# Performance work log

Hardware: AMD Instinct MI355X
Metric: run time of the kernel (lower is better)

Reference implementation:

```python
import jax, jax.numpy as jnp
import numpy as np

N_NODES = 100000
N_EDGES = 500000
FEAT = 128
HID = 256
N_ETYPES = 249
N_LINKS = 16384


def _lin_init(key, out_dim, in_dim, bias=True):
    k1, k2 = jax.random.split(key)
    bound = 1.0 / np.sqrt(in_dim)
    w = jax.random.uniform(k1, (out_dim, in_dim), jnp.float32, -bound, bound)
    if bias:
        b = jax.random.uniform(k2, (out_dim,), jnp.float32, -bound, bound)
        return w, b
    return w


def setup_inputs() -> dict:
    key = jax.random.key(0)
    ks = jax.random.split(key, 24)
    x = jax.random.normal(ks[0], (N_NODES, FEAT), jnp.float32)
    edge_index = jax.random.randint(ks[1], (2, N_EDGES), 0, N_NODES, jnp.int64)
    edge_type = jax.random.randint(ks[2], (N_EDGES,), 0, N_ETYPES, jnp.int64)
    src_idx = jax.random.randint(ks[3], (N_LINKS,), 0, N_NODES, jnp.int64)
    dst_idx = jax.random.randint(ks[4], (N_LINKS,), 0, N_NODES, jnp.int64)

    w_emb, b_emb = _lin_init(ks[5], HID, FEAT)
    edge_table = jax.random.normal(ks[6], (N_ETYPES, HID), jnp.float32)
    wl0, bl0 = _lin_init(ks[7], HID, HID)
    wr0 = _lin_init(ks[8], HID, HID, bias=False)
    we0, be0 = _lin_init(ks[9], HID, HID)
    wl1, bl1 = _lin_init(ks[10], HID, HID)
    wr1 = _lin_init(ks[11], HID, HID, bias=False)
    we1, be1 = _lin_init(ks[12], HID, HID)
    wp1, bp1 = _lin_init(ks[13], HID, 4 * HID)
    wp2, bp2 = _lin_init(ks[14], 1, HID)
    return dict(x=x, edge_index=edge_index, edge_type=edge_type,
                src_idx=src_idx, dst_idx=dst_idx,
                w_emb=w_emb, b_emb=b_emb, edge_table=edge_table,
                wl0=wl0, bl0=bl0, wr0=wr0, we0=we0, be0=be0,
                wl1=wl1, bl1=bl1, wr1=wr1, we1=we1, be1=be1,
                wp1=wp1, bp1=bp1, wp2=wp2, bp2=bp2)


def _sage_layer(h, src, dst, deg, wl, bl, wr):
    # mean aggregation over incoming edges + self loop (add_self_loops)
    nb_sum = jax.ops.segment_sum(h[src], dst, num_segments=N_NODES)  # [N,H]
    mean = (nb_sum + h) / (deg + 1.0)[:, None]
    return mean @ wl.T + bl + h @ wr.T  # lin_l(mean) + lin_r(x)


def reference(x, edge_index, edge_type, src_idx, dst_idx,
              w_emb, b_emb, edge_table,
              wl0, bl0, wr0, we0, be0,
              wl1, bl1, wr1, we1, be1,
              wp1, bp1, wp2, bp2):
    src, dst = edge_index[0], edge_index[1]
    deg = jax.ops.segment_sum(jnp.ones((src.shape[0],), jnp.float32), dst,
                              num_segments=N_NODES)  # in-degree (no self loop)
    h = x @ w_emb.T + b_emb  # node_embedding
    edge_emb = edge_table[edge_type]  # [E,H]
    # edge_lin outputs are discarded by SAGEConv (matches torch behavior)
    _ = edge_emb @ we0.T + be0
    _ = edge_emb @ we1.T + be1
    h = jax.nn.relu(_sage_layer(h, src, dst, deg, wl0, bl0, wr0))
    h = jax.nn.relu(_sage_layer(h, src, dst, deg, wl1, bl1, wr1))
    s, d = h[src_idx], h[dst_idx]
    combined = jnp.concatenate([s, d, s * d, jnp.abs(s - d)], axis=1)  # [B,4H]
    hidden = jax.nn.relu(combined @ wp1.T + bp1)
    logits = hidden @ wp2.T + bp2  # [B,1]
    return jax.nn.sigmoid(logits).squeeze()
```

## Files before the change

### kernel.cpp

```cpp
#include <hip/hip_runtime.h>
#include <hip/hip_bf16.h>
#include <cstdint>
#include <type_traits>

#define N_NODES 100000
#define N_EDGES 500000
#define FEAT 128
#define HID 256
#define N_LINKS 16384
#define BCAP 32

typedef __attribute__((ext_vector_type(8))) short short8;
typedef __attribute__((ext_vector_type(4))) float floatx4;
typedef __attribute__((ext_vector_type(16))) float floatx16;

__device__ __forceinline__ float ldf(const float* p) { return *p; }
__device__ __forceinline__ float ldf(const __hip_bfloat16* p) { return __bfloat162float(*p); }
__device__ __forceinline__ void stf(float* p, float v) { *p = v; }
__device__ __forceinline__ void stf(__hip_bfloat16* p, float v) { *p = __float2bfloat16(v); }

__device__ __forceinline__ void load4(const __hip_bfloat16* p, float v[4]) {
    const uint2 q = *(const uint2*)p;
    v[0] = __uint_as_float(q.x << 16);
    v[1] = __uint_as_float(q.x & 0xffff0000u);
    v[2] = __uint_as_float(q.y << 16);
    v[3] = __uint_as_float(q.y & 0xffff0000u);
}
__device__ __forceinline__ void store4(__hip_bfloat16* p, const float v[4]) {
    __hip_bfloat16 b[4];
    b[0] = __float2bfloat16(v[0]); b[1] = __float2bfloat16(v[1]);
    b[2] = __float2bfloat16(v[2]); b[3] = __float2bfloat16(v[3]);
    *(uint2*)p = *(const uint2*)b;
}

__device__ __forceinline__ void load8(const __hip_bfloat16* p, float v[8]) {
    const uint4 q = *(const uint4*)p;
    v[0] = __uint_as_float(q.x << 16);
    v[1] = __uint_as_float(q.x & 0xffff0000u);
    v[2] = __uint_as_float(q.y << 16);
    v[3] = __uint_as_float(q.y & 0xffff0000u);
    v[4] = __uint_as_float(q.z << 16);
    v[5] = __uint_as_float(q.z & 0xffff0000u);
    v[6] = __uint_as_float(q.w << 16);
    v[7] = __uint_as_float(q.w & 0xffff0000u);
}
__device__ __forceinline__ void store8(__hip_bfloat16* p, const float v[8]) {
    __hip_bfloat16 b[8];
    #pragma unroll
    for (int i = 0; i < 8; i++) b[i] = __float2bfloat16(v[i]);
    *(uint4*)p = *(const uint4*)b;
}

__device__ __forceinline__ void acc8(const uint4& q, float a[8]) {
    a[0] += __uint_as_float(q.x << 16);
    a[1] += __uint_as_float(q.x & 0xffff0000u);
    a[2] += __uint_as_float(q.y << 16);
    a[3] += __uint_as_float(q.y & 0xffff0000u);
    a[4] += __uint_as_float(q.z << 16);
    a[5] += __uint_as_float(q.z & 0xffff0000u);
    a[6] += __uint_as_float(q.w << 16);
    a[7] += __uint_as_float(q.w & 0xffff0000u);
}

__device__ __forceinline__ void gload_lds16(const short* g, short* lds) {
    __builtin_amdgcn_global_load_lds(
        reinterpret_cast<const __attribute__((address_space(1))) unsigned int*>(
            reinterpret_cast<uintptr_t>(g)),
        reinterpret_cast<__attribute__((address_space(3))) unsigned int*>(
            reinterpret_cast<uintptr_t>(lds)),
        16, 0, 0);
}

__device__ __forceinline__ int clampi(int v, int n) { return ((unsigned)v < (unsigned)n) ? v : 0; }


__global__ void zero_f32(float* p, int n) {
    int i = blockIdx.x * blockDim.x + threadIdx.x;
    if (i < n) p[i] = 0.0f;
}

__global__ void init_misc(int* __restrict__ deg, int* __restrict__ h0pad,
                          int* __restrict__ h1pad) {
    int i = blockIdx.x * blockDim.x + threadIdx.x;
    if (i < N_NODES) deg[i] = 0;
    if (i < 128) { h0pad[i] = 0; h1pad[i] = 0; }
}

__global__ void cvt_x(const float4* __restrict__ x, __hip_bfloat16* __restrict__ xb, int n4) {
    int i = blockIdx.x * blockDim.x + threadIdx.x;
    if (i >= n4) return;
    float4 v = x[i];
    float a[4] = {v.x, v.y, v.z, v.w};
    store4(&xb[(size_t)i * 4], a);
}

#define POF_EMB 0
#define POF_L0  32768
#define POF_R0  98304
#define POF_L1  163840
#define POF_R1  229376
#define WP_TOTAL 294912
#define WP1_N   262144
__global__ void cvt_wall(const float* __restrict__ w_emb, const float* __restrict__ wl0,
                         const float* __restrict__ wr0, const float* __restrict__ wl1,
                         const float* __restrict__ wr1, const float* __restrict__ wp1,
                         __hip_bfloat16* __restrict__ wbp, __hip_bfloat16* __restrict__ wbp1) {
    int i = blockIdx.x * blockDim.x + threadIdx.x;
    if (i < WP_TOTAL) {
        const float* src; int off, ks;
        if      (i < POF_L0) { src = w_emb; off = POF_EMB; ks = 128; }
        else if (i < POF_R0) { src = wl0;   off = POF_L0;  ks = 256; }
        else if (i < POF_L1) { src = wr0;   off = POF_R0;  ks = 256; }
        else if (i < POF_R1) { src = wl1;   off = POF_L1;  ks = 256; }
        else                 { src = wr1;   off = POF_R1;  ks = 256; }
        int o = i - off;
        int kseg = o >> 11;
        int rem  = o & 2047;
        int n = rem >> 3, j = rem & 7;
        wbp[i] = __float2bfloat16(src[n * ks + kseg * 8 + j]);
    } else if (i < WP_TOTAL + WP1_N) {
        int j = i - WP_TOTAL;
        wbp1[j] = __float2bfloat16(wp1[j]);
    }
}


__global__ void fill_buckets(const int* __restrict__ src, const int* __restrict__ dst,
                             int* __restrict__ deg, int* __restrict__ ebuf, int nE) {
    int e = blockIdx.x * blockDim.x + threadIdx.x;
    if (e >= nE) return;
    int d = clampi(dst[e], N_NODES);
    int pos = atomicAdd(&deg[d], 1);
    if (pos < BCAP) ebuf[d * BCAP + pos] = clampi(src[e], N_NODES);
}

__global__ void sort_rows(const int* __restrict__ deg, int* __restrict__ ebuf) {
    int n = blockIdx.x * blockDim.x + threadIdx.x;
    if (n >= N_NODES) return;
    int dg = deg[n]; if (dg > BCAP) dg = BCAP;
    int start = n * BCAP, end = start + dg;
    for (int i = start + 1; i < end; i++) {
        int key = ebuf[i];
        int j = i - 1;
        while (j >= start && ebuf[j] > key) { ebuf[j + 1] = ebuf[j]; j--; }
        ebuf[j + 1] = key;
    }
}


__global__ __launch_bounds__(256) void gather_agg(const __hip_bfloat16* __restrict__ h,
                                                  const int* __restrict__ deg,
                                                  const int* __restrict__ ebuf,
                                                  __hip_bfloat16* __restrict__ agg) {
    int wave = threadIdx.x >> 6, lane = threadIdx.x & 63;
    int half = lane >> 5, l32 = lane & 31;
    int n = blockIdx.x * 8 + wave * 2 + half;
    bool active = (n < N_NODES);
    int nn = active ? n : 0;
    int dg = active ? deg[nn] : 0;
    int dgc = dg > BCAP ? BCAP : dg;
    int start = nn * BCAP;
    int end = start + dgc;

    float acc[8];
    {
        float sv[8];
        load8(&h[(long long)nn * HID + l32 * 8], sv);
        #pragma unroll
        for (int k = 0; k < 8; k++) acc[k] = sv[k];
    }

    for (int e = start; e < end; e += 8) {
        int cnt = end - e;
        uint4 raw[8];
        #pragma unroll
        for (int i = 0; i < 8; i++) {
            int t = e + i; t = (t < end) ? t : (end - 1);
            int idx = ebuf[t];
            int s = (i < cnt) ? idx : N_NODES;
            raw[i] = *(const uint4*)&h[(long long)s * HID + l32 * 8];
        }
        #pragma unroll
        for (int i = 0; i < 8; i++) acc8(raw[i], acc);
    }

    float inv = 1.0f / (float)(dg + 1);
    #pragma unroll
    for (int k = 0; k < 8; k++) acc[k] *= inv;
    if (active) store8(&agg[(long long)n * HID + l32 * 8], acc);
}


template <int KS, bool DUAL, typename TC, bool RELU>
__global__ __launch_bounds__(256, 2) void gemm_kc(const __hip_bfloat16* __restrict__ A1,
                                                  const __hip_bfloat16* __restrict__ A2,
                                                  const __hip_bfloat16* __restrict__ Bp1,
                                                  const __hip_bfloat16* __restrict__ Bp2,
                                                  const float* __restrict__ bias,
                                                  TC* __restrict__ C, int M, int GX) {
    const int N = 256;
    const int NSTEP = (DUAL ? 2 : 1) * KS / 64;
    __shared__ __align__(16) short As[2][128 * 64];
    __shared__ __align__(16) short Bs[2][64 * 128];

    const int tid = threadIdx.x;
    const int w = tid >> 6, lane = tid & 63;
    const int half = lane >> 5, l32 = lane & 31;
    const int cg = blockIdx.y;

    const short* A1s = (const short*)A1;
    const short* A2s = (const short*)A2;
    const short* B1s = (const short*)Bp1;
    const short* B2s = (const short*)Bp2;

    const int NT = (M + 127) / 128;
    for (int tile = blockIdx.x; tile < NT; tile += GX) {
        const int row0 = tile * 128;

        auto stage = [&](int buf, int t) {
            const short* Asrc; const short* Bsrc; int kl;
            if (!DUAL || t < KS / 64) { Asrc = A1s; Bsrc = B1s; kl = t * 64; }
            else                      { Asrc = A2s; Bsrc = B2s; kl = t * 64 - KS; }
            #pragma unroll
            for (int i = 0; i < 4; i++) {
                int idx = i * 256 + tid;
                int row = idx >> 3, b16 = idx & 7;
                int gr = row0 + row; if (gr >= M) gr = M - 1;
                gload_lds16(Asrc + (size_t)gr * KS + kl + ((b16 ^ (row & 7)) * 8),
                            (short*)&As[buf][idx * 8]);
            }
            #pragma unroll
            for (int i = 0; i < 4; i++) {
                int idx = i * 256 + tid;
                int kseg = idx >> 7, col = idx & 127;
                gload_lds16(Bsrc + ((size_t)((kl >> 3) + kseg) * 256 + cg * 128 + col) * 8,
                            (short*)&Bs[buf][idx * 8]);
            }
        };

        floatx16 acc[4] = {};
        int cur = 0;
        stage(0, 0);
        __syncthreads();

        for (int t = 0; t < NSTEP; t++) {
            if (t + 1 < NSTEP) stage(cur ^ 1, t + 1);

            const int arow = w * 32 + l32;
            #pragma unroll
            for (int k16 = 0; k16 < 4; k16++) {
                int e = k16 * 2 + half;
                short8 a = *(const short8*)&As[cur][(arow * 8 + (e ^ (l32 & 7))) * 8];
                #pragma unroll
                for (int ct = 0; ct < 4; ct++) {
                    short8 b = *(const short8*)&Bs[cur][(e * 128 + ct * 32 + l32) * 8];
                    acc[ct] = __builtin_amdgcn_mfma_f32_32x32x16_bf16(a, b, acc[ct], 0, 0, 0);
                }
            }
            __syncthreads();
            cur ^= 1;
        }

        #pragma unroll
        for (int ct = 0; ct < 4; ct++) {
            int c = cg * 128 + ct * 32 + l32;
            float bc = bias[c];
            #pragma unroll
            for (int reg = 0; reg < 16; reg++) {
                int rr = row0 + w * 32 + (reg & 3) + 8 * (reg >> 2) + 4 * half;
                if (rr < M) {
                    float v = acc[ct][reg] + bc;
                    if (RELU) v = fmaxf(v, 0.0f);
                    stf(&C[(size_t)rr * N + c], v);
                }
            }
        }
    }
}


__device__ __forceinline__ short8 comb_frag(const __hip_bfloat16* __restrict__ h,
                                            int srow, int drow, int ka) {
    int seg = ka >> 8, off = ka & 255;
    const __hip_bfloat16* ps = &h[(size_t)srow * HID + off];
    const __hip_bfloat16* pd = &h[(size_t)drow * HID + off];
    if (seg == 0) return *(const short8*)ps;
    if (seg == 1) return *(const short8*)pd;
    float s[8], d[8];
    load8(ps, s);
    load8(pd, d);
    __hip_bfloat16 b[8];
    if (seg == 2) {
        #pragma unroll
        for (int j = 0; j < 8; j++) b[j] = __float2bfloat16(s[j] * d[j]);
    } else {
        #pragma unroll
        for (int j = 0; j < 8; j++) b[j] = __float2bfloat16(fabsf(s[j] - d[j]));
    }
    return *(const short8*)b;
}

template <int RT>
__global__ __launch_bounds__(256, 2) void pred_gemm(const __hip_bfloat16* __restrict__ h,
                                                    const int* __restrict__ src_idx,
                                                    const int* __restrict__ dst_idx,
                                                    const __hip_bfloat16* __restrict__ B1,
                                                    const float* __restrict__ bias,
                                                    float* __restrict__ C, int M, int K) {
    const int N = 256;
    const int SZ = 4 * 256 * 8;
    __shared__ __align__(16) short Bs[2][SZ];

    int w = threadIdx.x >> 6, lane = threadIdx.x & 63;
    int quad = lane >> 4, l16 = lane & 15;
    int wr = w >> 1, wc = w & 1;
    const int WROWS = RT * 16;
    int row0 = blockIdx.x * (2 * WROWS) + wr * WROWS;
    int colbase = wc * 128;

    const short* B1s = (const short*)B1;

    floatx4 acc[RT][8] = {};

    int r[RT], sidx[RT], didx[RT];
    #pragma unroll
    for (int i = 0; i < RT; i++) {
        int rr = row0 + i * 16 + l16;
        r[i] = rr < M ? rr : M - 1;
        sidx[i] = clampi(src_idx[r[i]], N_NODES);
        didx[i] = clampi(dst_idx[r[i]], N_NODES);
    }
    int scol = threadIdx.x;
    int ldsoff = (w * 64) * 8;

    short8 a1c[RT], a1n[RT];

    #pragma unroll
    for (int q = 0; q < 4; q++)
        gload_lds16(B1s + (size_t)scol * K + q * 8, &Bs[0][q * 256 * 8 + ldsoff]);
    {
        int ka = quad * 8;
        #pragma unroll
        for (int i = 0; i < RT; i++)
            a1c[i] = comb_frag(h, sidx[i], didx[i], ka);
    }
    __syncthreads();

    const int NK = K / 32;
    int cur = 0;
    for (int k = 0; k < NK; k++) {
        if (k + 1 < NK) {
            int k0n = (k + 1) * 32;
            #pragma unroll
            for (int q = 0; q < 4; q++)
                gload_lds16(B1s + (size_t)scol * K + k0n + q * 8,
                            &Bs[cur ^ 1][q * 256 * 8 + ldsoff]);
            int ka = k0n + quad * 8;
            #pragma unroll
            for (int i = 0; i < RT; i++)
                a1n[i] = comb_frag(h, sidx[i], didx[i], ka);
        }

        short8 b1[8];
        #pragma unroll
        for (int ct = 0; ct < 8; ct++) {
            int col = colbase + ct * 16 + l16;
            b1[ct] = *(const short8*)&Bs[cur][(quad * 256 + col) * 8];
        }
        #pragma unroll
        for (int i = 0; i < RT; i++)
            #pragma unroll
            for (int ct = 0; ct < 8; ct++)
                acc[i][ct] = __builtin_amdgcn_mfma_f32_16x16x32_bf16(a1c[i], b1[ct], acc[i][ct], 0, 0, 0);
        __syncthreads();
        cur ^= 1;
        #pragma unroll
        for (int i = 0; i < RT; i++) a1c[i] = a1n[i];
    }

    #pragma unroll
    for (int rt = 0; rt < RT; rt++) {
        #pragma unroll
        for (int ct = 0; ct < 8; ct++) {
            int c = colbase + ct * 16 + l16;
            float bc = bias[c];
            #pragma unroll
            for (int i = 0; i < 4; i++) {
                int rr = row0 + rt * 16 + quad * 4 + i;
                if (rr < M) {
                    float v = acc[rt][ct][i] + bc;
                    v = fmaxf(v, 0.0f);
                    C[(size_t)rr * N + c] = v;
                }
            }
        }
    }
}

__global__ __launch_bounds__(256) void pred_final(const float* __restrict__ hidden,
                                                  const float* __restrict__ wp2,
                                                  const float* __restrict__ bp2,
                                                  float* __restrict__ out) {
    int wave = threadIdx.x >> 6;
    int lane = threadIdx.x & 63;
    int row = blockIdx.x * 4 + wave;
    if (row >= N_LINKS) return;
    const float4 hv = *(const float4*)&hidden[(long long)row * HID + lane * 4];
    const float4 wv = *(const float4*)&wp2[lane * 4];
    float v = hv.x * wv.x + hv.y * wv.y + hv.z * wv.z + hv.w * wv.w;
    #pragma unroll
    for (int off = 32; off > 0; off >>= 1) v += __shfl_down(v, off, 64);
    if (lane == 0) out[row] = 1.0f / (1.0f + expf(-(v + bp2[0])));
}


extern "C" void kernel_launch(void* const* d_in, const int* in_sizes, int n_in,
                              void* d_out, int out_size, void* d_ws, size_t ws_size,
                              hipStream_t stream) {
    const float* x          = (const float*)d_in[0];
    const int*   edge_index = (const int*)d_in[1];
    const int*   e_src      = edge_index;
    const int*   e_dst      = edge_index + N_EDGES;
    const int*   src_idx    = (const int*)d_in[3];
    const int*   dst_idx    = (const int*)d_in[4];
    const float* w_emb      = (const float*)d_in[5];
    const float* b_emb      = (const float*)d_in[6];
    const float* wl0        = (const float*)d_in[8];
    const float* bl0        = (const float*)d_in[9];
    const float* wr0        = (const float*)d_in[10];
    const float* wl1        = (const float*)d_in[13];
    const float* bl1        = (const float*)d_in[14];
    const float* wr1        = (const float*)d_in[15];
    const float* wp1        = (const float*)d_in[18];
    const float* bp1        = (const float*)d_in[19];
    const float* wp2        = (const float*)d_in[20];
    const float* bp2        = (const float*)d_in[21];
    float* out = (float*)d_out;

    typedef __hip_bfloat16 bf16;
    const size_t NH  = (size_t)N_NODES * HID;
    const size_t NH1 = (size_t)(N_NODES + 1) * HID;

    char* p = (char*)d_ws;
    bf16* h0   = (bf16*)p;  p += NH1 * 2;
    bf16* h1   = (bf16*)p;  p += NH1 * 2;
    bf16* agg  = (bf16*)p;  p += NH * 2;
    bf16* xb   = (bf16*)p;  p += (size_t)N_NODES * FEAT * 2;
    bf16* wbp  = (bf16*)p;  p += (size_t)WP_TOTAL * 2;
    bf16* wbp1 = (bf16*)p;  p += (size_t)WP1_N * 2;
    p = (char*)(((uintptr_t)p + 255) & ~(uintptr_t)255);
    int* deg  = (int*)p; p += (size_t)N_NODES * 4;
    int* ebuf = (int*)p; p += (size_t)N_NODES * BCAP * 4;
    const size_t need = (size_t)(p - (char*)d_ws);

    if (ws_size < need) {
        zero_f32<<<(out_size + 255) / 256, 256, 0, stream>>>(out, out_size);
        return;
    }

    float* hidden = (float*)h1;

    init_misc<<<(N_NODES + 255) / 256, 256, 0, stream>>>(
        deg, (int*)(h0 + NH), (int*)(h1 + NH));
    fill_buckets<<<(N_EDGES + 255) / 256, 256, 0, stream>>>(e_src, e_dst, deg, ebuf, N_EDGES);
    sort_rows<<<(N_NODES + 255) / 256, 256, 0, stream>>>(deg, ebuf);

    cvt_x<<<((N_NODES * FEAT / 4) + 255) / 256, 256, 0, stream>>>((const float4*)x, xb, N_NODES * FEAT / 4);
    cvt_wall<<<((WP_TOTAL + WP1_N) + 255) / 256, 256, 0, stream>>>(
        w_emb, wl0, wr0, wl1, wr1, wp1, wbp, wbp1);

    const int GX = 256;
    dim3 pgrid(GX, 2);

    gemm_kc<128, false, bf16, false><<<pgrid, 256, 0, stream>>>(
        xb, nullptr, wbp + POF_EMB, nullptr, b_emb, h0, N_NODES, GX);

    gather_agg<<<(N_NODES + 7) / 8, 256, 0, stream>>>(h0, deg, ebuf, agg);
    gemm_kc<256, true, bf16, true><<<pgrid, 256, 0, stream>>>(
        agg, h0, wbp + POF_L0, wbp + POF_R0, bl0, h1, N_NODES, GX);

    gather_agg<<<(N_NODES + 7) / 8, 256, 0, stream>>>(h1, deg, ebuf, agg);
    gemm_kc<256, true, bf16, true><<<pgrid, 256, 0, stream>>>(
        agg, h1, wbp + POF_L1, wbp + POF_R1, bl1, h0, N_NODES, GX);

    pred_gemm<2><<<(N_LINKS + 63) / 64, 256, 0, stream>>>(
        h0, src_idx, dst_idx, wbp1, bp1, hidden, N_LINKS, 4 * HID);
    pred_final<<<N_LINKS / 4, 256, 0, stream>>>(hidden, wp2, bp2, out);
}
```

Before: 460.2 us.

## Repack predictor weights k-segmented and split pred_gemm across column groups

The predictor weight wp1 is now converted into the same k-segmented bf16 packed layout as the other weights, so each B stage becomes one coalesced 16-byte load per thread. pred_gemm is re-tiled: each block covers 64 rows by 64 columns, with a second grid dimension over four column groups and one 16-row tile per wave. This raises the block count from 256 to 1024, cuts LDS per block, and allows higher occupancy. The cost is that the gathered combined-feature A fragments are recomputed four times, once per column group.

Measured after the change: 468.3 us. About the same (+1.8%).

```diff
diff --git a/kernel.cpp b/kernel.cpp
--- a/kernel.cpp
+++ b/kernel.cpp
@@ -99,29 +99,26 @@
 #define POF_R0  98304
 #define POF_L1  163840
 #define POF_R1  229376
-#define WP_TOTAL 294912
-#define WP1_N   262144
+#define POF_P1  294912
+#define WP_ALL  557056
 __global__ void cvt_wall(const float* __restrict__ w_emb, const float* __restrict__ wl0,
                          const float* __restrict__ wr0, const float* __restrict__ wl1,
                          const float* __restrict__ wr1, const float* __restrict__ wp1,
-                         __hip_bfloat16* __restrict__ wbp, __hip_bfloat16* __restrict__ wbp1) {
+                         __hip_bfloat16* __restrict__ wbp) {
     int i = blockIdx.x * blockDim.x + threadIdx.x;
-    if (i < WP_TOTAL) {
-        const float* src; int off, ks;
-        if      (i < POF_L0) { src = w_emb; off = POF_EMB; ks = 128; }
-        else if (i < POF_R0) { src = wl0;   off = POF_L0;  ks = 256; }
-        else if (i < POF_L1) { src = wr0;   off = POF_R0;  ks = 256; }
-        else if (i < POF_R1) { src = wl1;   off = POF_L1;  ks = 256; }
-        else                 { src = wr1;   off = POF_R1;  ks = 256; }
-        int o = i - off;
-        int kseg = o >> 11;
-        int rem  = o & 2047;
-        int n = rem >> 3, j = rem & 7;
-        wbp[i] = __float2bfloat16(src[n * ks + kseg * 8 + j]);
-    } else if (i < WP_TOTAL + WP1_N) {
-        int j = i - WP_TOTAL;
-        wbp1[j] = __float2bfloat16(wp1[j]);
-    }
+    if (i >= WP_ALL) return;
+    const float* src; int off, ks;
+    if      (i < POF_L0) { src = w_emb; off = POF_EMB; ks = 128; }
+    else if (i < POF_R0) { src = wl0;   off = POF_L0;  ks = 256; }
+    else if (i < POF_L1) { src = wr0;   off = POF_R0;  ks = 256; }
+    else if (i < POF_R1) { src = wl1;   off = POF_L1;  ks = 256; }
+    else if (i < POF_P1) { src = wr1;   off = POF_R1;  ks = 256; }
+    else                 { src = wp1;   off = POF_P1;  ks = 1024; }
+    int o = i - off;
+    int kseg = o >> 11;
+    int rem  = o & 2047;
+    int n = rem >> 3, j = rem & 7;
+    wbp[i] = __float2bfloat16(src[n * ks + kseg * 8 + j]);
 }
 
 
@@ -300,99 +297,66 @@
     return *(const short8*)b;
 }
 
-template <int RT>
-__global__ __launch_bounds__(256, 2) void pred_gemm(const __hip_bfloat16* __restrict__ h,
+
+__global__ __launch_bounds__(256, 4) void pred_gemm(const __hip_bfloat16* __restrict__ h,
                                                     const int* __restrict__ src_idx,
                                                     const int* __restrict__ dst_idx,
-                                                    const __hip_bfloat16* __restrict__ B1,
+                                                    const __hip_bfloat16* __restrict__ Bp,
                                                     const float* __restrict__ bias,
-                                                    float* __restrict__ C, int M, int K) {
+                                                    float* __restrict__ C, int M) {
     const int N = 256;
-    const int SZ = 4 * 256 * 8;
-    __shared__ __align__(16) short Bs[2][SZ];
+    const int K = 1024;
+    __shared__ __align__(16) short Bs[2][4 * 64 * 8];
 
     int w = threadIdx.x >> 6, lane = threadIdx.x & 63;
     int quad = lane >> 4, l16 = lane & 15;
-    int wr = w >> 1, wc = w & 1;
-    const int WROWS = RT * 16;
-    int row0 = blockIdx.x * (2 * WROWS) + wr * WROWS;
-    int colbase = wc * 128;
-
-    const short* B1s = (const short*)B1;
-
-    floatx4 acc[RT][8] = {};
-
-    int r[RT], sidx[RT], didx[RT];
-    #pragma unroll
-    for (int i = 0; i < RT; i++) {
-        int rr = row0 + i * 16 + l16;
-        r[i] = rr < M ? rr : M - 1;
-        sidx[i] = clampi(src_idx[r[i]], N_NODES);
-        didx[i] = clampi(dst_idx[r[i]], N_NODES);
-    }
-    int scol = threadIdx.x;
-    int ldsoff = (w * 64) * 8;
-
-    short8 a1c[RT], a1n[RT];
-
-    #pragma unroll
-    for (int q = 0; q < 4; q++)
-        gload_lds16(B1s + (size_t)scol * K + q * 8, &Bs[0][q * 256 * 8 + ldsoff]);
-    {
-        int ka = quad * 8;
-        #pragma unroll
-        for (int i = 0; i < RT; i++)
-            a1c[i] = comb_frag(h, sidx[i], didx[i], ka);
-    }
+    int cg = blockIdx.y;
+    int row0 = blockIdx.x * 64 + w * 16;
+
+    const short* Bps = (const short*)Bp;
+
+    floatx4 acc[4] = {};
+
+    int rr = row0 + l16;
+    int r = rr < M ? rr : M - 1;
+    int sidx = clampi(src_idx[r], N_NODES);
+    int didx = clampi(dst_idx[r], N_NODES);
+
+    auto stageB = [&](int buf, int k0) {
+        gload_lds16(Bps + ((size_t)((k0 >> 3) + w) * 256 + cg * 64 + lane) * 8,
+                    (short*)&Bs[buf][(w * 64 + lane) * 8]);
+    };
+
+    short8 a1c, a1n;
+    stageB(0, 0);
+    a1c = comb_frag(h, sidx, didx, quad * 8);
     __syncthreads();
 
     const int NK = K / 32;
     int cur = 0;
     for (int k = 0; k < NK; k++) {
         if (k + 1 < NK) {
-            int k0n = (k + 1) * 32;
-            #pragma unroll
-            for (int q = 0; q < 4; q++)
-                gload_lds16(B1s + (size_t)scol * K + k0n + q * 8,
-                            &Bs[cur ^ 1][q * 256 * 8 + ldsoff]);
-            int ka = k0n + quad * 8;
-            #pragma unroll
-            for (int i = 0; i < RT; i++)
-                a1n[i] = comb_frag(h, sidx[i], didx[i], ka);
-        }
-
-        short8 b1[8];
-        #pragma unroll
-        for (int ct = 0; ct < 8; ct++) {
-            int col = colbase + ct * 16 + l16;
-            b1[ct] = *(const short8*)&Bs[cur][(quad * 256 + col) * 8];
-        }
-        #pragma unroll
-        for (int i = 0; i < RT; i++)
-            #pragma unroll
-            for (int ct = 0; ct < 8; ct++)
-                acc[i][ct] = __builtin_amdgcn_mfma_f32_16x16x32_bf16(a1c[i], b1[ct], acc[i][ct], 0, 0, 0);
+            stageB(cur ^ 1, (k + 1) * 32);
+            a1n = comb_frag(h, sidx, didx, (k + 1) * 32 + quad * 8);
+        }
+        #pragma unroll
+        for (int ct = 0; ct < 4; ct++) {
+            short8 b = *(const short8*)&Bs[cur][(quad * 64 + ct * 16 + l16) * 8];
+            acc[ct] = __builtin_amdgcn_mfma_f32_16x16x32_bf16(a1c, b, acc[ct], 0, 0, 0);
+        }
         __syncthreads();
         cur ^= 1;
-        #pragma unroll
-        for (int i = 0; i < RT; i++) a1c[i] = a1n[i];
+        a1c = a1n;
     }
 
     #pragma unroll
-    for (int rt = 0; rt < RT; rt++) {
-        #pragma unroll
-        for (int ct = 0; ct < 8; ct++) {
-            int c = colbase + ct * 16 + l16;
-            float bc = bias[c];
-            #pragma unroll
-            for (int i = 0; i < 4; i++) {
-                int rr = row0 + rt * 16 + quad * 4 + i;
-                if (rr < M) {
-                    float v = acc[rt][ct][i] + bc;
-                    v = fmaxf(v, 0.0f);
-                    C[(size_t)rr * N + c] = v;
-                }
-            }
+    for (int ct = 0; ct < 4; ct++) {
+        int c = cg * 64 + ct * 16 + l16;
+        float bc = bias[c];
+        #pragma unroll
+        for (int i = 0; i < 4; i++) {
+            int r2 = row0 + quad * 4 + i;
+            if (r2 < M) C[(size_t)r2 * N + c] = fmaxf(acc[ct][i] + bc, 0.0f);
         }
     }
 }
@@ -446,8 +410,7 @@
     bf16* h1   = (bf16*)p;  p += NH1 * 2;
     bf16* agg  = (bf16*)p;  p += NH * 2;
     bf16* xb   = (bf16*)p;  p += (size_t)N_NODES * FEAT * 2;
-    bf16* wbp  = (bf16*)p;  p += (size_t)WP_TOTAL * 2;
-    bf16* wbp1 = (bf16*)p;  p += (size_t)WP1_N * 2;
+    bf16* wbp  = (bf16*)p;  p += (size_t)WP_ALL * 2;
     p = (char*)(((uintptr_t)p + 255) & ~(uintptr_t)255);
     int* deg  = (int*)p; p += (size_t)N_NODES * 4;
     int* ebuf = (int*)p; p += (size_t)N_NODES * BCAP * 4;
@@ -466,8 +429,8 @@
     sort_rows<<<(N_NODES + 255) / 256, 256, 0, stream>>>(deg, ebuf);
 
     cvt_x<<<((N_NODES * FEAT / 4) + 255) / 256, 256, 0, stream>>>((const float4*)x, xb, N_NODES * FEAT / 4);
-    cvt_wall<<<((WP_TOTAL + WP1_N) + 255) / 256, 256, 0, stream>>>(
-        w_emb, wl0, wr0, wl1, wr1, wp1, wbp, wbp1);
+    cvt_wall<<<(WP_ALL + 255) / 256, 256, 0, stream>>>(
+        w_emb, wl0, wr0, wl1, wr1, wp1, wbp);
 
     const int GX = 256;
     dim3 pgrid(GX, 2);
@@ -483,7 +446,8 @@
     gemm_kc<256, true, bf16, true><<<pgrid, 256, 0, stream>>>(
         agg, h1, wbp + POF_L1, wbp + POF_R1, bl1, h0, N_NODES, GX);
 
-    pred_gemm<2><<<(N_LINKS + 63) / 64, 256, 0, stream>>>(
-        h0, src_idx, dst_idx, wbp1, bp1, hidden, N_LINKS, 4 * HID);
+    dim3 pgrid2(N_LINKS / 64, 4);
+    pred_gemm<<<pgrid2, 256, 0, stream>>>(
+        h0, src_idx, dst_idx, wbp + POF_P1, bp1, hidden, N_LINKS);
     pred_final<<<N_LINKS / 4, 256, 0, stream>>>(hidden, wp2, bp2, out);
 }
```
